# Performance work log

Measured on AMD Instinct MI355X. Metric: run time of the kernel, lower is better.

The kernel has to match this reference:

```python
import jax, jax.numpy as jnp
import numpy as np

IH = IW = 1024          # image size (iH, iW)
NMS_CAND = 1000         # dup_attrs['nms_candidates']
NMS_THR = 0.65          # dup_attrs['nms_thr']
MAX_SEGS = 100          # max_segs


def _mask_to_box(masks):
    # masks: [N, H, W] bool -> xyxy float boxes [N, 4] in pixel coords
    N, H, W = masks.shape
    rows = masks.any(axis=2)            # [N, H]
    cols = masks.any(axis=1)            # [N, W]
    x1 = jnp.argmax(cols, axis=1)
    x2 = W - jnp.argmax(cols[:, ::-1], axis=1)
    y1 = jnp.argmax(rows, axis=1)
    y2 = H - jnp.argmax(rows[:, ::-1], axis=1)
    return jnp.stack([x1, y1, x2, y2], axis=-1).astype(jnp.float32)


def _box_iou(b):
    # b: [K, 4] xyxy -> pairwise IoU [K, K]
    x1, y1, x2, y2 = b[:, 0], b[:, 1], b[:, 2], b[:, 3]
    area = (x2 - x1) * (y2 - y1)
    ix1 = jnp.maximum(x1[:, None], x1[None, :])
    iy1 = jnp.maximum(y1[:, None], y1[None, :])
    ix2 = jnp.minimum(x2[:, None], x2[None, :])
    iy2 = jnp.minimum(y2[:, None], y2[None, :])
    inter = jnp.clip(ix2 - ix1, 0.0) * jnp.clip(iy2 - iy1, 0.0)
    union = area[:, None] + area[None, :] - inter
    return inter / jnp.maximum(union, 1e-9)


def _greedy_nms_keep(iou, thr):
    # boxes assumed pre-sorted by descending score; returns keep mask [K]
    k = iou.shape[0]
    idx = jnp.arange(k)

    def body(i, keep):
        sup = keep[i] & (iou[i] > thr) & (idx > i)
        return keep & ~sup

    return jax.lax.fori_loop(0, k, body, jnp.ones((k,), dtype=bool))


def setup_inputs() -> dict:
    key = jax.random.key(0)
    k1, k2 = jax.random.split(key)
    cls_logits = jax.random.normal(k1, (300, 81), dtype=jnp.float32)
    seg_logits = jax.random.normal(k2, (300, 200, 200), dtype=jnp.float32)
    return {"cls_logits": cls_logits, "seg_logits": seg_logits}


def reference(cls_logits, seg_logits):
    N, fH, fW = seg_logits.shape
    C = cls_logits.shape[1] - 1  # last class is background/no-object

    # mask thresholding + emptiness flag (filtering replaced by score masking)
    pred_masks = seg_logits > 0                              # [N, fH, fW]
    non_empty = pred_masks.reshape(N, -1).sum(axis=1) > 0    # [N]

    # mask -> box for NMS
    boxes = _mask_to_box(pred_masks)                         # [N, 4]

    # sigmoid scoring over (feat, class); empty masks get score -1 (never picked)
    scores = jax.nn.sigmoid(cls_logits[:, :-1])              # [N, C]
    scores = jnp.where(non_empty[:, None], scores, -1.0).reshape(-1)  # [N*C]
    feat_ids = jnp.repeat(jnp.arange(N), C)                  # [N*C]
    labels = jnp.tile(jnp.arange(C), N)                      # [N*C]

    # top nms_candidates (scores sorted descending)
    k = min(NMS_CAND, N * C)
    cand_scores, cand_ids = jax.lax.top_k(scores, k)
    cand_feats = feat_ids[cand_ids]
    cand_labels = labels[cand_ids]
    cand_boxes = boxes[cand_feats]

    # batched (class-aware) NMS: offset boxes per label
    offset = cand_labels.astype(jnp.float32)[:, None] * (float(max(fH, fW)) + 1.0)
    iou = _box_iou(cand_boxes + offset)
    keep = _greedy_nms_keep(iou, NMS_THR) & (cand_scores >= 0.0)

    # keep top max_segs among survivors
    kept_scores = jnp.where(keep, cand_scores, -jnp.inf)
    sel_scores, sel = jax.lax.top_k(kept_scores, MAX_SEGS)
    sel_feats = cand_feats[sel]
    sel_labels = cand_labels[sel]

    # upsample selected mask logits to image size and threshold
    sel_logits = seg_logits[sel_feats]                       # [M, fH, fW]
    maps = jax.image.resize(sel_logits, (MAX_SEGS, IH, IW), method='bilinear')
    out_masks = maps > 0                                     # [M, iH, iW] bool
    batch_ids = jnp.zeros((MAX_SEGS,), dtype=jnp.int32)

    return sel_labels, out_masks, sel_scores, batch_ids
```

## Files before the change

kernel.cpp:

```cpp
#include <hip/hip_runtime.h>
#include <cstdint>
#include <cstddef>

typedef unsigned int u32;
typedef unsigned long long u64;
typedef float vf4 __attribute__((ext_vector_type(4)));

#define NF 300
#define NCLS 80
#define NCLS1 81
#define FH 200
#define FW 200
#define PIX 40000
#define NC 24000
#define KCAND 1000
#define CAP 4096
#define NBINS 65536
#define MAXSEG 100
#define OUT_MASK_OFF 100
#define OUT_SCORE_OFF 104857700
#define OUT_BATCH_OFF 104857800
#define NEG_BIG -3.3895313892515355e38f
#define RYC 8

#define WS_HIST      0u
#define WS_KEYS      262144u
#define WS_COLLECT   454144u
#define WS_CNT       486912u
#define WS_BOXES     486928u
#define WS_CLAB      496928u
#define WS_CFEAT     500928u
#define WS_CSCORE    504928u
#define WS_CBOX      508928u
#define WS_ROWBITS   524928u
#define WS_SELFEAT   656128u
#define WS_WTAB      656528u

__device__ __forceinline__ u32 ord32_r3(float f) {
  u32 b = __float_as_uint(f);
  return (b & 0x80000000u) ? ~b : (b | 0x80000000u);
}
__device__ __forceinline__ float unord32_r3(u32 o) {
  u32 b = (o & 0x80000000u) ? (o & 0x7FFFFFFFu) : ~o;
  return __uint_as_float(b);
}

__global__ void r3_init_wtab(u32* __restrict__ hist, u32* __restrict__ cnts,
                             float4* __restrict__ wtab) {
  int i = blockIdx.x * 256 + threadIdx.x;
  hist[i] = 0u;
  if (i < 4) cnts[i] = 0u;
  if (i < 1024) {
    float s = __fsub_rn(__fmul_rn((float)i + 0.5f, 0.1953125f), 0.5f);
    int j0 = (int)floorf(s);
    int j1 = j0 + 1;
    float w0 = fmaxf(0.f, __fsub_rn(1.f, fabsf(__fsub_rn(s, (float)j0))));
    float w1 = fmaxf(0.f, __fsub_rn(1.f, fabsf(__fsub_rn(s, (float)j1))));
    bool in0 = (j0 >= 0) && (j0 < FH);
    bool in1 = (j1 >= 0) && (j1 < FH);
    float tot = __fadd_rn(in0 ? w0 : 0.f, in1 ? w1 : 0.f);
    float w0n = in0 ? (w0 / tot) : 0.f;
    float w1n = in1 ? (w1 / tot) : 0.f;
    wtab[i] = make_float4(w0n, w1n, (float)max(j0, 0), (float)min(j1, FH - 1));
  }
}

__global__ void r3_boxes_scores(const float* __restrict__ seg, const float* __restrict__ cls,
                                float4* __restrict__ boxes, u64* __restrict__ keys,
                                u32* __restrict__ hist) {
  __shared__ int sminx[256], sminy[256], smaxx[256], smaxy[256];
  int n = blockIdx.x, t = threadIdx.x;
  const float4* img = (const float4*)(seg + (size_t)n * PIX);
  int minx = FW, miny = FH, maxx = -1, maxy = -1;
  for (int q = t; q < PIX / 4; q += 256) {
    float4 v = img[q];
    int p = q * 4;
    int y = p / FW;
    int x = p - y * FW;
    if (v.x > 0.f) { minx = min(minx, x);     maxx = max(maxx, x);     miny = min(miny, y); maxy = max(maxy, y); }
    if (v.y > 0.f) { minx = min(minx, x + 1); maxx = max(maxx, x + 1); miny = min(miny, y); maxy = max(maxy, y); }
    if (v.z > 0.f) { minx = min(minx, x + 2); maxx = max(maxx, x + 2); miny = min(miny, y); maxy = max(maxy, y); }
    if (v.w > 0.f) { minx = min(minx, x + 3); maxx = max(maxx, x + 3); miny = min(miny, y); maxy = max(maxy, y); }
  }
  sminx[t] = minx; sminy[t] = miny; smaxx[t] = maxx; smaxy[t] = maxy;
  __syncthreads();
  for (int s = 128; s > 0; s >>= 1) {
    if (t < s) {
      sminx[t] = min(sminx[t], sminx[t + s]);
      sminy[t] = min(sminy[t], sminy[t + s]);
      smaxx[t] = max(smaxx[t], smaxx[t + s]);
      smaxy[t] = max(smaxy[t], smaxy[t + s]);
    }
    __syncthreads();
  }
  bool ne = smaxx[0] >= 0;
  if (t == 0) {
    float4 b;
    if (ne) b = make_float4((float)sminx[0], (float)sminy[0], (float)(smaxx[0] + 1), (float)(smaxy[0] + 1));
    else    b = make_float4(0.f, 0.f, (float)FW, (float)FH);
    boxes[n] = b;
  }
  if (t < NCLS) {
    float sc;
    if (ne) {
      float lg = cls[n * NCLS1 + t];
      sc = 1.0f / (1.0f + expf(-lg));
    } else {
      sc = -1.0f;
    }
    u32 o = ord32_r3(sc);
    u32 i = (u32)(n * NCLS + t);
    keys[i] = ((u64)o << 32) | (u64)(0xFFFFFFFFu - i);
    atomicAdd(&hist[o >> 16], 1u);
  }
}

__global__ void r3_thresh(const u32* __restrict__ hist, u32* __restrict__ cnts) {
  __shared__ u32 s[1024];
  int t = threadIdx.x;
  u32 sum = 0;
  const u32* hp = hist + t * 64;
  for (int b = 0; b < 64; b++) sum += hp[b];
  s[t] = sum;
  __syncthreads();
  for (int off = 1; off < 1024; off <<= 1) {
    u32 v = s[t];
    u32 o = (t + off < 1024) ? s[t + off] : 0u;
    __syncthreads();
    s[t] = v + o;
    __syncthreads();
  }
  u32 sufnext = (t < 1023) ? s[t + 1] : 0u;
  if (s[t] >= (u32)KCAND && sufnext < (u32)KCAND) {
    u32 run = sufnext;
    u32 B = (u32)(t * 64);
    for (int b = 63; b >= 0; b--) {
      run += hist[t * 64 + b];
      if (run >= (u32)KCAND) { B = (u32)(t * 64 + b); break; }
    }
    cnts[1] = B;
  }
}

__global__ void r3_collect(const u64* __restrict__ keys, const u32* __restrict__ cnts,
                           u64* __restrict__ collect, u32* __restrict__ counter) {
  int i = blockIdx.x * 256 + threadIdx.x;
  if (i >= NC) return;
  u64 k = keys[i];
  if ((u32)(k >> 48) >= cnts[1]) {
    u32 pos = atomicAdd(counter, 1u);
    if (pos < CAP) collect[pos] = k;
  }
}

__global__ void r3_rank(const u64* __restrict__ collect, const u32* __restrict__ cnts,
                        const float4* __restrict__ boxes,
                        int* __restrict__ clab, int* __restrict__ cfeat,
                        float* __restrict__ cscore, float4* __restrict__ cbox) {
  __shared__ u64 sk[CAP];
  int M = min((int)cnts[0], CAP);
  int t = threadIdx.x;
  for (int j = t; j < M; j += 64) sk[j] = collect[j];
  __syncthreads();
  for (int j = blockIdx.x * 64 + t; j < M; j += 64 * 16) {
    u64 mykey = sk[j];
    int r = 0;
    for (int k = 0; k < M; k++) r += (sk[k] > mykey) ? 1 : 0;
    if (r < KCAND) {
      u32 idx = 0xFFFFFFFFu - (u32)(mykey & 0xFFFFFFFFull);
      int n = (int)idx / NCLS, c = (int)idx - n * NCLS;
      clab[r] = c;
      cfeat[r] = n;
      cscore[r] = unord32_r3((u32)(mykey >> 32));
      float4 b = boxes[n];
      float off = (float)c * 201.0f;
      cbox[r] = make_float4(b.x + off, b.y + off, b.z + off, b.w + off);
    }
  }
}

__global__ void r3_iou(const float4* __restrict__ cbox, u64* __restrict__ rowbits) {
  int i = blockIdx.x;
  int lane = threadIdx.x;
  float4 bi = make_float4(0.f, 0.f, 0.f, 0.f);
  float ai = 0.f;
  if (i < KCAND) { bi = cbox[i]; ai = (bi.z - bi.x) * (bi.w - bi.y); }
  for (int ch = 0; ch < 16; ch++) {
    int j = ch * 64 + lane;
    bool pred = false;
    if (i < KCAND && j < KCAND && j > i) {
      float4 bj = cbox[j];
      float aj = (bj.z - bj.x) * (bj.w - bj.y);
      float ix1 = fmaxf(bi.x, bj.x), iy1 = fmaxf(bi.y, bj.y);
      float ix2 = fminf(bi.z, bj.z), iy2 = fminf(bi.w, bj.w);
      float inter = fmaxf(ix2 - ix1, 0.f) * fmaxf(iy2 - iy1, 0.f);
      float uni = ai + aj - inter;
      float iou = inter / fmaxf(uni, 1e-9f);
      pred = iou > 0.65f;
    }
    u64 m = __ballot(pred);
    if (lane == 0) rowbits[(size_t)i * 16 + ch] = m;
  }
}

__global__ void r3_nms_sel(const u64* __restrict__ rowbits, const float* __restrict__ cscore,
                           const int* __restrict__ clab, const int* __restrict__ cfeat,
                           float* __restrict__ out, int* __restrict__ selfeat) {
  __shared__ u64 sup[16];
  __shared__ u64 keep[16];
  __shared__ u64 sk[KCAND];
  int t = threadIdx.x;
  if (t < 16) sup[t] = 0ull;
  __syncthreads();
  for (int c = 0; c < 16; c++) {
    if (t < 64) {
      int L = t;
      u64 r = rowbits[(size_t)(c * 64 + L) * 16 + c];
      u64 s = sup[c];
      u64 k = 0ull;
      #pragma unroll 4
      for (int b = 0; b < 64; b++) {
        u64 rb = __shfl(r, b, 64);
        if (!((s >> b) & 1ull)) { s |= rb; k |= (1ull << b); }
      }
      if (L == 0) { sup[c] = s; keep[c] = k; }
      if (L > c && L < 16) {
        u64 acc = sup[L];
        for (int b = 0; b < 64; b++)
          if ((k >> b) & 1ull) acc |= rowbits[(size_t)(c * 64 + b) * 16 + L];
        sup[L] = acc;
      }
    }
    __syncthreads();
  }
  for (int j = t; j < KCAND; j += 1024) {
    bool kp = ((keep[j >> 6] >> (j & 63)) & 1ull) != 0ull;
    float sc = cscore[j];
    u32 hi = (kp && sc >= 0.f) ? ord32_r3(sc) : 0u;
    sk[j] = ((u64)hi << 32) | (u64)(0xFFFFFFFFu - (u32)j);
  }
  __syncthreads();
  if (t < KCAND) {
    u64 my = sk[t];
    int r = 0;
    for (int k = 0; k < KCAND; k++) r += (sk[k] > my) ? 1 : 0;
    if (r < MAXSEG) {
      u32 hi = (u32)(my >> 32);
      float oscore = (hi == 0u) ? NEG_BIG : unord32_r3(hi);
      oscore = fmaxf(oscore, NEG_BIG);
      out[r] = (float)clab[t];
      out[OUT_SCORE_OFF + r] = oscore;
      out[OUT_BATCH_OFF + r] = 0.0f;
      selfeat[r] = cfeat[t];
    }
  }
}

__global__ void __launch_bounds__(256) r3_resize(const float* __restrict__ seg,
                                                 const int* __restrict__ selfeat,
                                                 const float4* __restrict__ wtab,
                                                 float* __restrict__ outm) {
  __shared__ float4 swx[1024];
  __shared__ float srow[4][FW];
  int t = threadIdx.x;
  int yb = blockIdx.x * RYC, slot = blockIdx.y;
  int feat = selfeat[slot];
  const float* img = seg + (size_t)feat * PIX;
  #pragma unroll
  for (int k = 0; k < 4; k++) swx[t + 256 * k] = wtab[t + 256 * k];
  int ylo = (int)wtab[yb].z;
  int yhi = (int)wtab[yb + RYC - 1].w;
  int nr = yhi - ylo + 1;
  for (int e = t; e < nr * FW; e += 256) {
    int rr = e / FW, cc = e - rr * FW;
    srow[rr][cc] = img[(ylo + rr) * FW + cc];
  }
  __syncthreads();
  int xb = t * 4;
  float4 wxa = swx[xb], wxb = swx[xb + 1], wxc = swx[xb + 2], wxd = swx[xb + 3];
  int xa0 = (int)wxa.z, xa1 = (int)wxa.w;
  int xb0 = (int)wxb.z, xb1 = (int)wxb.w;
  int xc0 = (int)wxc.z, xc1 = (int)wxc.w;
  int xd0 = (int)wxd.z, xd1 = (int)wxd.w;
  float* obase = outm + (size_t)slot * 1048576 + (size_t)yb * 1024 + xb;
  #pragma unroll
  for (int r = 0; r < RYC; r++) {
    int y = yb + r;
    float4 wy = wtab[y];
    const float* r0 = srow[(int)wy.z - ylo];
    const float* r1 = srow[(int)wy.w - ylo];
    float wy0 = wy.x, wy1 = wy.y;
    float ta0 = __fmaf_rn(wy1, r1[xa0], __fmul_rn(wy0, r0[xa0]));
    float ta1 = __fmaf_rn(wy1, r1[xa1], __fmul_rn(wy0, r0[xa1]));
    float va  = __fmaf_rn(wxa.y, ta1, __fmul_rn(wxa.x, ta0));
    float tb0 = __fmaf_rn(wy1, r1[xb0], __fmul_rn(wy0, r0[xb0]));
    float tb1 = __fmaf_rn(wy1, r1[xb1], __fmul_rn(wy0, r0[xb1]));
    float vb  = __fmaf_rn(wxb.y, tb1, __fmul_rn(wxb.x, tb0));
    float tc0 = __fmaf_rn(wy1, r1[xc0], __fmul_rn(wy0, r0[xc0]));
    float tc1 = __fmaf_rn(wy1, r1[xc1], __fmul_rn(wy0, r0[xc1]));
    float vc  = __fmaf_rn(wxc.y, tc1, __fmul_rn(wxc.x, tc0));
    float td0 = __fmaf_rn(wy1, r1[xd0], __fmul_rn(wy0, r0[xd0]));
    float td1 = __fmaf_rn(wy1, r1[xd1], __fmul_rn(wy0, r0[xd1]));
    float vd  = __fmaf_rn(wxd.y, td1, __fmul_rn(wxd.x, td0));
    vf4 res;
    res.x = (va > 0.0f) ? 1.0f : 0.0f;
    res.y = (vb > 0.0f) ? 1.0f : 0.0f;
    res.z = (vc > 0.0f) ? 1.0f : 0.0f;
    res.w = (vd > 0.0f) ? 1.0f : 0.0f;
    __builtin_nontemporal_store(res, (vf4*)(obase + (size_t)r * 1024));
  }
}

extern "C" void kernel_launch(void* const* d_in, const int* in_sizes, int n_in,
                              void* d_out, int out_size, void* d_ws, size_t ws_size,
                              hipStream_t stream) {
  const float* cls = (const float*)d_in[0];
  const float* seg = (const float*)d_in[1];
  float* out = (float*)d_out;
  char* ws = (char*)d_ws;

  u32* hist      = (u32*)(ws + WS_HIST);
  u64* keys      = (u64*)(ws + WS_KEYS);
  u64* collect   = (u64*)(ws + WS_COLLECT);
  u32* cnts      = (u32*)(ws + WS_CNT);
  float4* boxes  = (float4*)(ws + WS_BOXES);
  int* clab      = (int*)(ws + WS_CLAB);
  int* cfeat     = (int*)(ws + WS_CFEAT);
  float* cscore  = (float*)(ws + WS_CSCORE);
  float4* cbox   = (float4*)(ws + WS_CBOX);
  u64* rowbits   = (u64*)(ws + WS_ROWBITS);
  int* selfeat   = (int*)(ws + WS_SELFEAT);
  float4* wtab   = (float4*)(ws + WS_WTAB);

  r3_init_wtab<<<dim3(NBINS / 256), dim3(256), 0, stream>>>(hist, cnts, wtab);
  r3_boxes_scores<<<dim3(NF), dim3(256), 0, stream>>>(seg, cls, boxes, keys, hist);
  r3_thresh<<<dim3(1), dim3(1024), 0, stream>>>(hist, cnts);
  r3_collect<<<dim3((NC + 255) / 256), dim3(256), 0, stream>>>(keys, cnts, collect, &cnts[0]);
  r3_rank<<<dim3(16), dim3(64), 0, stream>>>(collect, cnts, boxes, clab, cfeat, cscore, cbox);
  r3_iou<<<dim3(1024), dim3(64), 0, stream>>>(cbox, rowbits);
  r3_nms_sel<<<dim3(1), dim3(1024), 0, stream>>>(rowbits, cscore, clab, cfeat, out, selfeat);
  r3_resize<<<dim3(1024 / RYC, MAXSEG), dim3(256), 0, stream>>>(seg, selfeat, wtab, out + OUT_MASK_OFF);
}
```

Baseline: 656.5 us.

## Split NMS and selection kernels, double resize row chunk, drop shared x-weight table

Result: no change. 660.3 us (+0.6%).

```diff
diff --git a/kernel.cpp b/kernel.cpp
--- a/kernel.cpp
+++ b/kernel.cpp
@@ -21,7 +21,7 @@
 #define OUT_SCORE_OFF 104857700
 #define OUT_BATCH_OFF 104857800
 #define NEG_BIG -3.3895313892515355e38f
-#define RYC 8
+#define RYC 16
 
 #define WS_HIST      0u
 #define WS_KEYS      262144u
@@ -35,6 +35,7 @@
 #define WS_ROWBITS   524928u
 #define WS_SELFEAT   656128u
 #define WS_WTAB      656528u
+#define WS_KEEP      672912u
 
 __device__ __forceinline__ u32 ord32_r3(float f) {
   u32 b = __float_as_uint(f);
@@ -203,55 +204,65 @@
   }
 }
 
-__global__ void r3_nms_sel(const u64* __restrict__ rowbits, const float* __restrict__ cscore,
-                           const int* __restrict__ clab, const int* __restrict__ cfeat,
-                           float* __restrict__ out, int* __restrict__ selfeat) {
+__global__ void r3_nms(const u64* __restrict__ rowbits, u64* __restrict__ keepout) {
   __shared__ u64 sup[16];
   __shared__ u64 keep[16];
+  int t = threadIdx.x;
+  if (t < 16) sup[t] = 0ull;
+  __syncthreads();
+  for (int c = 0; c < 16; c++) {
+    int L = t;
+    u64 r = rowbits[(size_t)(c * 64 + L) * 16 + c];
+    u64 s = sup[c];
+    u64 k = 0ull;
+    #pragma unroll 4
+    for (int b = 0; b < 64; b++) {
+      u64 rb = __shfl(r, b, 64);
+      if (!((s >> b) & 1ull)) { s |= rb; k |= (1ull << b); }
+    }
+    if (L == 0) { sup[c] = s; keep[c] = k; }
+    if (L > c && L < 16) {
+      u64 acc = sup[L];
+      #pragma unroll
+      for (int b = 0; b < 64; b++) {
+        u64 v = rowbits[(size_t)(c * 64 + b) * 16 + L];
+        if ((k >> b) & 1ull) acc |= v;
+      }
+      sup[L] = acc;
+    }
+    __syncthreads();
+  }
+  if (t < 16) keepout[t] = keep[t];
+}
+
+__global__ void r3_sel(const u64* __restrict__ keepbits, const float* __restrict__ cscore,
+                       const int* __restrict__ clab, const int* __restrict__ cfeat,
+                       float* __restrict__ out, int* __restrict__ selfeat) {
   __shared__ u64 sk[KCAND];
-  int t = threadIdx.x;
-  if (t < 16) sup[t] = 0ull;
-  __syncthreads();
-  for (int c = 0; c < 16; c++) {
-    if (t < 64) {
-      int L = t;
-      u64 r = rowbits[(size_t)(c * 64 + L) * 16 + c];
-      u64 s = sup[c];
-      u64 k = 0ull;
-      #pragma unroll 4
-      for (int b = 0; b < 64; b++) {
-        u64 rb = __shfl(r, b, 64);
-        if (!((s >> b) & 1ull)) { s |= rb; k |= (1ull << b); }
-      }
-      if (L == 0) { sup[c] = s; keep[c] = k; }
-      if (L > c && L < 16) {
-        u64 acc = sup[L];
-        for (int b = 0; b < 64; b++)
-          if ((k >> b) & 1ull) acc |= rowbits[(size_t)(c * 64 + b) * 16 + L];
-        sup[L] = acc;
-      }
-    }
-    __syncthreads();
-  }
-  for (int j = t; j < KCAND; j += 1024) {
-    bool kp = ((keep[j >> 6] >> (j & 63)) & 1ull) != 0ull;
+  __shared__ u64 kb[16];
+  int t = threadIdx.x;
+  if (t < 16) kb[t] = keepbits[t];
+  __syncthreads();
+  for (int j = t; j < KCAND; j += 64) {
+    bool kp = ((kb[j >> 6] >> (j & 63)) & 1ull) != 0ull;
     float sc = cscore[j];
     u32 hi = (kp && sc >= 0.f) ? ord32_r3(sc) : 0u;
     sk[j] = ((u64)hi << 32) | (u64)(0xFFFFFFFFu - (u32)j);
   }
   __syncthreads();
-  if (t < KCAND) {
-    u64 my = sk[t];
+  int j = blockIdx.x * 64 + t;
+  if (j < KCAND) {
+    u64 my = sk[j];
     int r = 0;
     for (int k = 0; k < KCAND; k++) r += (sk[k] > my) ? 1 : 0;
     if (r < MAXSEG) {
       u32 hi = (u32)(my >> 32);
       float oscore = (hi == 0u) ? NEG_BIG : unord32_r3(hi);
       oscore = fmaxf(oscore, NEG_BIG);
-      out[r] = (float)clab[t];
+      out[r] = (float)clab[j];
       out[OUT_SCORE_OFF + r] = oscore;
       out[OUT_BATCH_OFF + r] = 0.0f;
-      selfeat[r] = cfeat[t];
+      selfeat[r] = cfeat[j];
     }
   }
 }
@@ -260,14 +271,12 @@
                                                  const int* __restrict__ selfeat,
                                                  const float4* __restrict__ wtab,
                                                  float* __restrict__ outm) {
-  __shared__ float4 swx[1024];
-  __shared__ float srow[4][FW];
+  __shared__ float srow[6][FW];
   int t = threadIdx.x;
   int yb = blockIdx.x * RYC, slot = blockIdx.y;
   int feat = selfeat[slot];
   const float* img = seg + (size_t)feat * PIX;
-  #pragma unroll
-  for (int k = 0; k < 4; k++) swx[t + 256 * k] = wtab[t + 256 * k];
+  float4 wxa = wtab[t * 4], wxb = wtab[t * 4 + 1], wxc = wtab[t * 4 + 2], wxd = wtab[t * 4 + 3];
   int ylo = (int)wtab[yb].z;
   int yhi = (int)wtab[yb + RYC - 1].w;
   int nr = yhi - ylo + 1;
@@ -277,7 +286,6 @@
   }
   __syncthreads();
   int xb = t * 4;
-  float4 wxa = swx[xb], wxb = swx[xb + 1], wxc = swx[xb + 2], wxd = swx[xb + 3];
   int xa0 = (int)wxa.z, xa1 = (int)wxa.w;
   int xb0 = (int)wxb.z, xb1 = (int)wxb.w;
   int xc0 = (int)wxc.z, xc1 = (int)wxc.w;
@@ -331,6 +339,7 @@
   u64* rowbits   = (u64*)(ws + WS_ROWBITS);
   int* selfeat   = (int*)(ws + WS_SELFEAT);
   float4* wtab   = (float4*)(ws + WS_WTAB);
+  u64* keepbits  = (u64*)(ws + WS_KEEP);
 
   r3_init_wtab<<<dim3(NBINS / 256), dim3(256), 0, stream>>>(hist, cnts, wtab);
   r3_boxes_scores<<<dim3(NF), dim3(256), 0, stream>>>(seg, cls, boxes, keys, hist);
@@ -338,6 +347,7 @@
   r3_collect<<<dim3((NC + 255) / 256), dim3(256), 0, stream>>>(keys, cnts, collect, &cnts[0]);
   r3_rank<<<dim3(16), dim3(64), 0, stream>>>(collect, cnts, boxes, clab, cfeat, cscore, cbox);
   r3_iou<<<dim3(1024), dim3(64), 0, stream>>>(cbox, rowbits);
-  r3_nms_sel<<<dim3(1), dim3(1024), 0, stream>>>(rowbits, cscore, clab, cfeat, out, selfeat);
+  r3_nms<<<dim3(1), dim3(64), 0, stream>>>(rowbits, keepbits);
+  r3_sel<<<dim3(16), dim3(64), 0, stream>>>(keepbits, cscore, clab, cfeat, out, selfeat);
   r3_resize<<<dim3(1024 / RYC, MAXSEG), dim3(256), 0, stream>>>(seg, selfeat, wtab, out + OUT_MASK_OFF);
 }
```
